# Performance work log

Measured on AMD Instinct MI355X. Metric: run time of the kernel, lower is better.

## Reference

```python
import jax, jax.numpy as jnp
import numpy as np

N = 6000        # nodes
F_IN = 300      # input feature dim
HID = 128       # per-head hidden dim
H = 8           # heads
NEG_INF = -9e15 # mask value used by dense GAT
ALPHA = 0.2     # LeakyReLU slope

# NOTE: dropout (p=0.6) is applied in torch only when training=True; this
# reference implements eval mode, so all dropouts are identity.

def setup_inputs() -> dict:
    key = jax.random.key(0)
    k1, k2, k3, k4, k5, k6 = jax.random.split(key, 6)
    x = jax.random.normal(k1, (N, F_IN), dtype=jnp.float32)
    # sparse-ish 0/1 dense adjacency with self-loops (row-normalizable mask)
    adj = (jax.random.uniform(k2, (N, N)) < 0.05).astype(jnp.float32)
    adj = jnp.maximum(adj, jnp.eye(N, dtype=jnp.float32))
    # per-head params: W ~ xavier_uniform, a ~ xavier_uniform ([2*HID, 1])
    def xavier(k, shape):
        fan_in, fan_out = shape[-2], shape[-1]
        lim = jnp.sqrt(6.0 / (fan_in + fan_out)).astype(jnp.float32)
        return jax.random.uniform(k, shape, jnp.float32, -lim, lim)
    W_heads = xavier(k3, (H, F_IN, HID))          # 8 attention heads
    a_heads = xavier(k4, (H, 2 * HID, 1))
    W_out = xavier(k5, (H * HID, HID))            # final GAT layer
    a_out = xavier(k6, (2 * HID, 1))
    return {"x": x, "adj": adj, "W_heads": W_heads, "a_heads": a_heads,
            "W_out": W_out, "a_out": a_out}


def _masked_softmax(e, adj):
    # attention = softmax over rows, restricted to adj > 0
    return jax.nn.softmax(jnp.where(adj > 0, e, NEG_INF), axis=-1)


def reference(x, adj, W_heads, a_heads, W_out, a_out):
    # ---- multi-head dense GAT layer (concat=True) ----
    Wh = jnp.einsum('nf,hfo->hno', x, W_heads)                    # [H,N,O]
    a1 = a_heads[:, :HID, 0]                                      # [H,O]
    a2 = a_heads[:, HID:, 0]                                      # [H,O]
    f1 = jnp.einsum('hno,ho->hn', Wh, a1)                         # [H,N]
    f2 = jnp.einsum('hno,ho->hn', Wh, a2)                         # [H,N]
    e = jax.nn.leaky_relu(f1[:, :, None] + f2[:, None, :], ALPHA) # [H,N,N]
    attn = _masked_softmax(e, adj[None])                          # [H,N,N]
    h = jax.nn.elu(jnp.einsum('hnm,hmo->hno', attn, Wh))          # [H,N,O]
    hcat = jnp.transpose(h, (1, 0, 2)).reshape(N, H * HID)        # [N,H*O]

    # ---- final GAT layer (concat=False, no elu) ----
    Wh2 = hcat @ W_out                                            # [N,O]
    g1 = (Wh2 @ a_out[:HID]).squeeze(-1)                          # [N]
    g2 = (Wh2 @ a_out[HID:]).squeeze(-1)                          # [N]
    e2 = jax.nn.leaky_relu(g1[:, None] + g2[None, :], ALPHA)      # [N,N]
    attn2 = _masked_softmax(e2, adj)                              # [N,N]
    out = attn2 @ Wh2                                             # [N,O]
    return out
```

## Files before the change

### kernel.cpp

```cpp
#include <hip/hip_runtime.h>
#include <hip/hip_fp16.h>
#include <math.h>

#define N 6000
#define FIN 300
#define HID 128
#define NH 8
#define ALPHA 0.2f
#define NBR_CAP 512
#define KSPLIT 4

typedef unsigned short u16;
typedef unsigned int u32;
typedef short bf16x8 __attribute__((ext_vector_type(8)));
typedef float f32x4 __attribute__((ext_vector_type(4)));

static __device__ __forceinline__ u16 f2bf(float f) {
    u32 u = __float_as_uint(f);
    u32 r = (u + 0x7fff + ((u >> 16) & 1)) >> 16;
    return (u16)r;
}
static __device__ __forceinline__ u16 f2h(float f) {
    return __half_as_ushort(__float2half(f));
}

__global__ void build_nbr(const float* __restrict__ adj,
                          u16* __restrict__ nbr,
                          int* __restrict__ ncnt) {
    int n = blockIdx.x;
    int t = threadIdx.x;
    int lane = t & 63, w = t >> 6;
    __shared__ u16 lbuf[4][256];
    __shared__ int wc[4];
    const int seg = N / 4;
    int start = w * seg, end = start + seg;
    const float* row = adj + (size_t)n * N;
    int cnt = 0;
    for (int base = start; base < end; base += 256) {
        int m0 = base + 4 * lane;
        float4 v = make_float4(0.f, 0.f, 0.f, 0.f);
        if (m0 < end) v = *(const float4*)(row + m0);
#pragma unroll
        for (int c = 0; c < 4; c++) {
            float vc = (c == 0) ? v.x : (c == 1) ? v.y : (c == 2) ? v.z : v.w;
            bool p = vc > 0.5f;
            unsigned long long mask = __ballot(p);
            if (p) {
                int pos = cnt + __popcll(mask & ((1ull << lane) - 1ull));
                if (pos < 256) lbuf[w][pos] = (u16)(m0 + c);
            }
            cnt += __popcll(mask);
        }
    }
    if (cnt > 256) cnt = 256;
    if (lane == 0) wc[w] = cnt;
    __syncthreads();
    int offset = 0;
    for (int i = 0; i < w; i++) offset += wc[i];
    for (int i = lane; i < cnt; i += 64) {
        int idx = offset + i;
        if (idx < NBR_CAP) nbr[(size_t)n * NBR_CAP + idx] = lbuf[w][i];
    }
    if (t == 0) {
        int total = wc[0] + wc[1] + wc[2] + wc[3];
        ncnt[n] = total < NBR_CAP ? total : NBR_CAP;
    }
}

__global__ void gemm_wh(const float* __restrict__ x,
                        const float* __restrict__ W,
                        const float* __restrict__ a_heads,
                        u16* __restrict__ Whb,
                        float* __restrict__ f1, float* __restrict__ f2) {
    int h = blockIdx.y;
    int n0 = blockIdx.x * 64;
    __shared__ float xs[64][21];
    __shared__ float bs[20][128];
    int t = threadIdx.x;
    int tx = t & 31, ty = t >> 5;
    float acc[8][4] = {};
    for (int k0 = 0; k0 < FIN; k0 += 20) {
        for (int i = t; i < 64 * 20; i += 256) {
            int r = i / 20, c = i - r * 20;
            int n = n0 + r;
            xs[r][c] = (n < N) ? x[(size_t)n * FIN + k0 + c] : 0.f;
        }
        for (int i = t; i < 20 * 128; i += 256) {
            int r = i >> 7, c = i & 127;
            bs[r][c] = W[((size_t)h * FIN + (k0 + r)) * HID + c];
        }
        __syncthreads();
#pragma unroll
        for (int kk = 0; kk < 20; kk++) {
            float b[4];
#pragma unroll
            for (int j = 0; j < 4; j++) b[j] = bs[kk][tx * 4 + j];
#pragma unroll
            for (int i = 0; i < 8; i++) {
                float a = xs[ty * 8 + i][kk];
#pragma unroll
                for (int j = 0; j < 4; j++) acc[i][j] += a * b[j];
            }
        }
        __syncthreads();
    }
    float a1c[4], a2c[4];
#pragma unroll
    for (int j = 0; j < 4; j++) {
        a1c[j] = a_heads[(size_t)h * 2 * HID + tx * 4 + j];
        a2c[j] = a_heads[(size_t)h * 2 * HID + HID + tx * 4 + j];
    }
    for (int i = 0; i < 8; i++) {
        int n = n0 + ty * 8 + i;
        float s1 = 0.f, s2 = 0.f;
#pragma unroll
        for (int j = 0; j < 4; j++) { s1 += acc[i][j] * a1c[j]; s2 += acc[i][j] * a2c[j]; }
        for (int d = 1; d <= 16; d <<= 1) { s1 += __shfl_xor(s1, d); s2 += __shfl_xor(s2, d); }
        if (n < N) {
            size_t ro = ((size_t)h * N + n) * HID + tx * 4;
            ushort4 b4;
            b4.x = f2bf(acc[i][0]); b4.y = f2bf(acc[i][1]);
            b4.z = f2bf(acc[i][2]); b4.w = f2bf(acc[i][3]);
            *(ushort4*)(Whb + ro) = b4;
            if (tx == 0) { f1[h * N + n] = s1; f2[h * N + n] = s2; }
        }
    }
}

__global__ void prep_wout(const float* __restrict__ W_out,
                          u16* __restrict__ WoT) {
    int idx = blockIdx.x * 256 + threadIdx.x;
    int k = idx & 1023, c = idx >> 10;
    WoT[(size_t)c * 1024 + k] = f2bf(W_out[(size_t)k * HID + c]);
}

__global__ void gat1(const u16* __restrict__ Whb,
                     const float* __restrict__ f1, const float* __restrict__ f2,
                     const u16* __restrict__ nbr,
                     const int* __restrict__ ncnt,
                     u16* __restrict__ hcatb) {
    int bid = blockIdx.x;
    int h = bid / N, n = bid - h * N;
    int t = threadIdx.x;
    int s = t >> 4, op = t & 15;
    int cnt = ncnt[n];
    const u16* lst = nbr + (size_t)n * NBR_CAP;
    __shared__ float2 wm[NBR_CAP];
    __shared__ float accl[16][16][9];
    __shared__ float swl[16];

    float f1c = f1[h * N + n];
    for (int i = t; i < cnt; i += 256) {
        int m = lst[i];
        float z = f1c + f2[h * N + m];
        z = (z >= 0.f) ? z : ALPHA * z;
        wm[i] = make_float2(__expf(z), __uint_as_float((u32)m << 8));
    }
    __syncthreads();

    const char* base = (const char*)(Whb + (size_t)h * N * HID) + (op << 4);
    float acc[8] = {};
    float sw = 0.f;
    int j = s;
    for (; j + 16 < cnt; j += 32) {
        float2 p0 = wm[j];
        float2 p1 = wm[j + 16];
        const uint4 va = *(const uint4*)(base + __float_as_uint(p0.y));
        const uint4 vb = *(const uint4*)(base + __float_as_uint(p1.y));
        float w0 = p0.x, w1 = p1.x;
        acc[0] += w0 * __uint_as_float(va.x << 16);
        acc[1] += w0 * __uint_as_float(va.x);
        acc[2] += w0 * __uint_as_float(va.y << 16);
        acc[3] += w0 * __uint_as_float(va.y);
        acc[4] += w0 * __uint_as_float(va.z << 16);
        acc[5] += w0 * __uint_as_float(va.z);
        acc[6] += w0 * __uint_as_float(va.w << 16);
        acc[7] += w0 * __uint_as_float(va.w);
        acc[0] += w1 * __uint_as_float(vb.x << 16);
        acc[1] += w1 * __uint_as_float(vb.x);
        acc[2] += w1 * __uint_as_float(vb.y << 16);
        acc[3] += w1 * __uint_as_float(vb.y);
        acc[4] += w1 * __uint_as_float(vb.z << 16);
        acc[5] += w1 * __uint_as_float(vb.z);
        acc[6] += w1 * __uint_as_float(vb.w << 16);
        acc[7] += w1 * __uint_as_float(vb.w);
        sw += w0 + w1;
    }
    if (j < cnt) {
        float2 p0 = wm[j];
        const uint4 va = *(const uint4*)(base + __float_as_uint(p0.y));
        float w0 = p0.x;
        acc[0] += w0 * __uint_as_float(va.x << 16);
        acc[1] += w0 * __uint_as_float(va.x);
        acc[2] += w0 * __uint_as_float(va.y << 16);
        acc[3] += w0 * __uint_as_float(va.y);
        acc[4] += w0 * __uint_as_float(va.z << 16);
        acc[5] += w0 * __uint_as_float(va.z);
        acc[6] += w0 * __uint_as_float(va.w << 16);
        acc[7] += w0 * __uint_as_float(va.w);
        sw += w0;
    }
#pragma unroll
    for (int c = 0; c < 8; c++) accl[s][op][c] = acc[c];
    if (op == 0) swl[s] = sw;
    __syncthreads();

    if (t < 128) {
        int c = t;
        float r = 0.f;
#pragma unroll
        for (int k = 0; k < 16; k++) r += accl[k][c >> 3][c & 7];
        float swt = 0.f;
#pragma unroll
        for (int k = 0; k < 16; k++) swt += swl[k];
        r /= swt;
        r = (r > 0.f) ? r : expm1f(r);
        hcatb[(size_t)n * (NH * HID) + h * HID + c] = f2bf(r);
    }
}

__global__ __launch_bounds__(256)
void gemm_out_mfma(const u16* __restrict__ hcatb,
                   const u16* __restrict__ WoT,
                   float* __restrict__ partial) {
    int n0 = blockIdx.x * 64;
    int ks = blockIdx.y;
    int t = threadIdx.x;
    int lane = t & 63, wid = t >> 6;
    int l4 = lane >> 4, lr = lane & 15;

    __shared__ u16 Bt[128][128];

    f32x4 acc[8];
#pragma unroll
    for (int ct = 0; ct < 8; ct++) acc[ct] = (f32x4){0.f, 0.f, 0.f, 0.f};

    int arow = n0 + 16 * wid + lr;
    const u16* asrc = hcatb + (size_t)arow * (NH * HID);
    bool avalid = (arow < N);

    for (int half = 0; half < 2; half++) {
        int kbeg = ks * 256 + half * 128;
        {
            int c = t >> 1, sh = t & 1;
            const u16* src = WoT + (size_t)c * 1024 + kbeg + sh * 64;
            int cx = (c & 7) << 3;
            uint4 v[8];
#pragma unroll
            for (int j = 0; j < 8; j++) v[j] = ((const uint4*)src)[j];
#pragma unroll
            for (int j = 0; j < 8; j++)
                *(uint4*)&Bt[c][(sh * 64 + 8 * j) ^ cx] = v[j];
        }
        __syncthreads();
#pragma unroll
        for (int kst = 0; kst < 4; kst++) {
            int kb = kst * 32 + 8 * l4;
            bf16x8 a = {0, 0, 0, 0, 0, 0, 0, 0};
            if (avalid) a = *(const bf16x8*)(asrc + kbeg + kb);
#pragma unroll
            for (int ct = 0; ct < 8; ct++) {
                int brow = 16 * ct + lr;
                bf16x8 b = *(const bf16x8*)&Bt[brow][kb ^ ((brow & 7) << 3)];
                acc[ct] = __builtin_amdgcn_mfma_f32_16x16x32_bf16(a, b, acc[ct], 0, 0, 0);
            }
        }
        __syncthreads();
    }
    float* pout = partial + (size_t)ks * N * HID;
#pragma unroll
    for (int reg = 0; reg < 4; reg++) {
        int n = n0 + 16 * wid + 4 * l4 + reg;
        if (n < N) {
#pragma unroll
            for (int ct = 0; ct < 8; ct++)
                pout[(size_t)n * HID + 16 * ct + lr] = acc[ct][reg];
        }
    }
}

__global__ void reduce_wh2(const float* __restrict__ partial,
                           const float* __restrict__ a_out,
                           u16* __restrict__ Wh2h,
                           float* __restrict__ g1, float* __restrict__ g2) {
    int idx = blockIdx.x * 256 + threadIdx.x;
    float4 v = *(const float4*)(partial + 4 * (size_t)idx);
#pragma unroll
    for (int s = 1; s < KSPLIT; s++) {
        const float4 q = *(const float4*)(partial + (size_t)s * N * HID + 4 * (size_t)idx);
        v.x += q.x; v.y += q.y; v.z += q.z; v.w += q.w;
    }
    ushort4 h4;
    h4.x = f2h(v.x); h4.y = f2h(v.y); h4.z = f2h(v.z); h4.w = f2h(v.w);
    *(ushort4*)(Wh2h + 4 * (size_t)idx) = h4;

    int row = idx >> 5, cg = idx & 31;
    float p1 = v.x * a_out[4 * cg] + v.y * a_out[4 * cg + 1]
             + v.z * a_out[4 * cg + 2] + v.w * a_out[4 * cg + 3];
    float p2 = v.x * a_out[HID + 4 * cg] + v.y * a_out[HID + 4 * cg + 1]
             + v.z * a_out[HID + 4 * cg + 2] + v.w * a_out[HID + 4 * cg + 3];
    for (int d = 1; d <= 16; d <<= 1) { p1 += __shfl_xor(p1, d); p2 += __shfl_xor(p2, d); }
    if ((threadIdx.x & 31) == 0) { g1[row] = p1; g2[row] = p2; }
}

__global__ void gat2(const u16* __restrict__ Wh2h,
                     const float* __restrict__ g1, const float* __restrict__ g2,
                     const u16* __restrict__ nbr,
                     const int* __restrict__ ncnt,
                     float* __restrict__ out) {
    int n = blockIdx.x, t = threadIdx.x;
    int s = t >> 4, op = t & 15;
    int cnt = ncnt[n];
    const u16* lst = nbr + (size_t)n * NBR_CAP;
    __shared__ float2 wm[NBR_CAP];
    __shared__ float accl[16][16][9];
    __shared__ float swl[16];

    float g1c = g1[n];
    for (int i = t; i < cnt; i += 256) {
        int m = lst[i];
        float z = g1c + g2[m];
        z = (z >= 0.f) ? z : ALPHA * z;
        wm[i] = make_float2(__expf(z), __uint_as_float((u32)m << 8));
    }
    __syncthreads();

    const char* base = (const char*)Wh2h + (op << 4);
    float acc[8] = {};
    float sw = 0.f;
    int j = s;
    for (; j + 16 < cnt; j += 32) {
        float2 p0 = wm[j];
        float2 p1 = wm[j + 16];
        const uint4 va = *(const uint4*)(base + __float_as_uint(p0.y));
        const uint4 vb = *(const uint4*)(base + __float_as_uint(p1.y));
        float w0 = p0.x, w1 = p1.x;
        acc[0] += w0 * __half2float(__ushort_as_half((u16)(va.x & 0xffff)));
        acc[1] += w0 * __half2float(__ushort_as_half((u16)(va.x >> 16)));
        acc[2] += w0 * __half2float(__ushort_as_half((u16)(va.y & 0xffff)));
        acc[3] += w0 * __half2float(__ushort_as_half((u16)(va.y >> 16)));
        acc[4] += w0 * __half2float(__ushort_as_half((u16)(va.z & 0xffff)));
        acc[5] += w0 * __half2float(__ushort_as_half((u16)(va.z >> 16)));
        acc[6] += w0 * __half2float(__ushort_as_half((u16)(va.w & 0xffff)));
        acc[7] += w0 * __half2float(__ushort_as_half((u16)(va.w >> 16)));
        acc[0] += w1 * __half2float(__ushort_as_half((u16)(vb.x & 0xffff)));
        acc[1] += w1 * __half2float(__ushort_as_half((u16)(vb.x >> 16)));
        acc[2] += w1 * __half2float(__ushort_as_half((u16)(vb.y & 0xffff)));
        acc[3] += w1 * __half2float(__ushort_as_half((u16)(vb.y >> 16)));
        acc[4] += w1 * __half2float(__ushort_as_half((u16)(vb.z & 0xffff)));
        acc[5] += w1 * __half2float(__ushort_as_half((u16)(vb.z >> 16)));
        acc[6] += w1 * __half2float(__ushort_as_half((u16)(vb.w & 0xffff)));
        acc[7] += w1 * __half2float(__ushort_as_half((u16)(vb.w >> 16)));
        sw += w0 + w1;
    }
    if (j < cnt) {
        float2 p0 = wm[j];
        const uint4 va = *(const uint4*)(base + __float_as_uint(p0.y));
        float w0 = p0.x;
        acc[0] += w0 * __half2float(__ushort_as_half((u16)(va.x & 0xffff)));
        acc[1] += w0 * __half2float(__ushort_as_half((u16)(va.x >> 16)));
        acc[2] += w0 * __half2float(__ushort_as_half((u16)(va.y & 0xffff)));
        acc[3] += w0 * __half2float(__ushort_as_half((u16)(va.y >> 16)));
        acc[4] += w0 * __half2float(__ushort_as_half((u16)(va.z & 0xffff)));
        acc[5] += w0 * __half2float(__ushort_as_half((u16)(va.z >> 16)));
        acc[6] += w0 * __half2float(__ushort_as_half((u16)(va.w & 0xffff)));
        acc[7] += w0 * __half2float(__ushort_as_half((u16)(va.w >> 16)));
        sw += w0;
    }
#pragma unroll
    for (int c = 0; c < 8; c++) accl[s][op][c] = acc[c];
    if (op == 0) swl[s] = sw;
    __syncthreads();

    if (t < 128) {
        int c = t;
        float r = 0.f;
#pragma unroll
        for (int k = 0; k < 16; k++) r += accl[k][c >> 3][c & 7];
        float swt = 0.f;
#pragma unroll
        for (int k = 0; k < 16; k++) swt += swl[k];
        out[(size_t)n * HID + c] = r / swt;
    }
}

extern "C" void kernel_launch(void* const* d_in, const int* in_sizes, int n_in,
                              void* d_out, int out_size, void* d_ws, size_t ws_size,
                              hipStream_t stream) {
    const float* x       = (const float*)d_in[0];
    const float* adj     = (const float*)d_in[1];
    const float* W_heads = (const float*)d_in[2];
    const float* a_heads = (const float*)d_in[3];
    const float* W_out   = (const float*)d_in[4];
    const float* a_out   = (const float*)d_in[5];
    float* out = (float*)d_out;

    char* wsb = (char*)d_ws;
    size_t off = 0;
    auto alloc = [&](size_t bytes) {
        void* p = wsb + off;
        off += (bytes + 255) & ~(size_t)255;
        return p;
    };
    float* partial = (float*)alloc(sizeof(float) * (size_t)KSPLIT * N * HID);
    u16*   Whb  = (u16*)  alloc(sizeof(u16)   * (size_t)NH * N * HID);
    u16*   hcatb= (u16*)  alloc(sizeof(u16)   * (size_t)N * NH * HID);
    u16*   WoT  = (u16*)  alloc(sizeof(u16)   * (size_t)HID * 1024);
    u16*   Wh2h = (u16*)  alloc(sizeof(u16)   * (size_t)N * HID);
    float* f1   = (float*)alloc(sizeof(float) * (size_t)NH * N);
    float* f2   = (float*)alloc(sizeof(float) * (size_t)NH * N);
    float* g1   = (float*)alloc(sizeof(float) * (size_t)N);
    float* g2   = (float*)alloc(sizeof(float) * (size_t)N);
    u16* nbr    = (u16*)  alloc(sizeof(u16)   * (size_t)N * NBR_CAP);
    int* ncnt   = (int*)  alloc(sizeof(int)   * (size_t)N);

    hipLaunchKernelGGL(build_nbr, dim3(N), dim3(256), 0, stream, adj, nbr, ncnt);
    hipLaunchKernelGGL(gemm_wh, dim3((N + 63) / 64, NH), dim3(256), 0, stream,
                       x, W_heads, a_heads, Whb, f1, f2);
    hipLaunchKernelGGL(prep_wout, dim3(512), dim3(256), 0, stream, W_out, WoT);
    hipLaunchKernelGGL(gat1, dim3(NH * N), dim3(256), 0, stream, Whb, f1, f2, nbr, ncnt, hcatb);
    hipLaunchKernelGGL(gemm_out_mfma, dim3((N + 63) / 64, KSPLIT), dim3(256), 0, stream,
                       hcatb, WoT, partial);
    hipLaunchKernelGGL(reduce_wh2, dim3(N * HID / 4 / 256), dim3(256), 0, stream,
                       partial, a_out, Wh2h, g1, g2);
    hipLaunchKernelGGL(gat2, dim3(N), dim3(256), 0, stream, Wh2h, g1, g2, nbr, ncnt, out);
}
```

Before: 321.2 us.

## Move first-layer projection GEMM to bf16 MFMA with precomputed attention vectors

Replaces the fp32 SIMT GEMM for x·W_heads with a bf16 MFMA kernel over padded, pre-converted and transposed operands held in swizzled LDS. The f1/f2 attention logits are now computed separately as x·(W·a) through a small precomputed vector per head, so they no longer depend on the GEMM epilogue. The W_out prep is folded into one combined prep kernel. This aims to cut first-layer GEMM time, at the cost of extra conversion passes, an additional launch and bf16 rounding of the x input.

```diff
diff --git a/kernel.cpp b/kernel.cpp
--- a/kernel.cpp
+++ b/kernel.cpp
@@ -9,6 +9,7 @@
 #define ALPHA 0.2f
 #define NBR_CAP 512
 #define KSPLIT 4
+#define KPAD 384
 
 typedef unsigned short u16;
 typedef unsigned int u32;
@@ -67,71 +68,134 @@
     }
 }
 
-__global__ void gemm_wh(const float* __restrict__ x,
-                        const float* __restrict__ W,
-                        const float* __restrict__ a_heads,
-                        u16* __restrict__ Whb,
-                        float* __restrict__ f1, float* __restrict__ f2) {
+__global__ void prep_all(const float* __restrict__ x,
+                         const float* __restrict__ W,
+                         const float* __restrict__ W_out,
+                         const float* __restrict__ a_heads,
+                         u16* __restrict__ xb,
+                         u16* __restrict__ WbT,
+                         u16* __restrict__ WoT,
+                         float* __restrict__ av1, float* __restrict__ av2) {
+    int bid = blockIdx.x, t = threadIdx.x;
+    if (bid < 9000) {
+        int idx = bid * 256 + t;
+        int n = idx / KPAD, k = idx - n * KPAD;
+        xb[idx] = (k < FIN) ? f2bf(x[(size_t)n * FIN + k]) : (u16)0;
+    } else if (bid < 9000 + 1536) {
+        int idx = (bid - 9000) * 256 + t;
+        int k = idx % KPAD;
+        int c = (idx / KPAD) & 127;
+        int h = idx / (KPAD * HID);
+        WbT[idx] = (k < FIN) ? f2bf(W[((size_t)h * FIN + k) * HID + c]) : (u16)0;
+    } else if (bid < 9000 + 1536 + 512) {
+        int idx = (bid - 9000 - 1536) * 256 + t;
+        int k = idx & 1023, c = idx >> 10;
+        WoT[idx] = f2bf(W_out[(size_t)k * HID + c]);
+    } else {
+        int h = bid - (9000 + 1536 + 512);
+        __shared__ float a1s[HID], a2s[HID];
+        if (t < HID) {
+            a1s[t] = a_heads[(size_t)h * 2 * HID + t];
+            a2s[t] = a_heads[(size_t)h * 2 * HID + HID + t];
+        }
+        __syncthreads();
+        for (int f = t; f < 320; f += 256) {
+            float s1 = 0.f, s2 = 0.f;
+            if (f < FIN) {
+                const float* wr = W + ((size_t)h * FIN + f) * HID;
+#pragma unroll 4
+                for (int o = 0; o < HID; o++) { s1 += wr[o] * a1s[o]; s2 += wr[o] * a2s[o]; }
+            }
+            av1[h * 320 + f] = s1;
+            av2[h * 320 + f] = s2;
+        }
+    }
+}
+
+__global__ void calc_f(const float* __restrict__ x,
+                       const float* __restrict__ av1, const float* __restrict__ av2,
+                       float* __restrict__ f1, float* __restrict__ f2) {
+    int n = blockIdx.x, t = threadIdx.x;
+    int lane = t & 63, w = t >> 6;
+    __shared__ float xsh[320];
+    for (int i = t; i < 320; i += 256)
+        xsh[i] = (i < FIN) ? x[(size_t)n * FIN + i] : 0.f;
+    __syncthreads();
+#pragma unroll
+    for (int hh = 0; hh < 2; hh++) {
+        int h = 2 * w + hh;
+        const float* a1 = av1 + h * 320;
+        const float* a2 = av2 + h * 320;
+        float s1 = 0.f, s2 = 0.f;
+#pragma unroll
+        for (int i = 0; i < 5; i++) {
+            float xv = xsh[lane + 64 * i];
+            s1 += xv * a1[lane + 64 * i];
+            s2 += xv * a2[lane + 64 * i];
+        }
+        for (int d = 1; d <= 32; d <<= 1) { s1 += __shfl_xor(s1, d); s2 += __shfl_xor(s2, d); }
+        if (lane == 0) { f1[h * N + n] = s1; f2[h * N + n] = s2; }
+    }
+}
+
+__global__ __launch_bounds__(256)
+void gemm_wh_mfma(const u16* __restrict__ xb,
+                  const u16* __restrict__ WbT,
+                  u16* __restrict__ Whb) {
+    int n0 = blockIdx.x * 64;
     int h = blockIdx.y;
-    int n0 = blockIdx.x * 64;
-    __shared__ float xs[64][21];
-    __shared__ float bs[20][128];
     int t = threadIdx.x;
-    int tx = t & 31, ty = t >> 5;
-    float acc[8][4] = {};
-    for (int k0 = 0; k0 < FIN; k0 += 20) {
-        for (int i = t; i < 64 * 20; i += 256) {
-            int r = i / 20, c = i - r * 20;
-            int n = n0 + r;
-            xs[r][c] = (n < N) ? x[(size_t)n * FIN + k0 + c] : 0.f;
-        }
-        for (int i = t; i < 20 * 128; i += 256) {
-            int r = i >> 7, c = i & 127;
-            bs[r][c] = W[((size_t)h * FIN + (k0 + r)) * HID + c];
+    int lane = t & 63, wid = t >> 6;
+    int l4 = lane >> 4, lr = lane & 15;
+
+    __shared__ u16 Bt[128][128];
+
+    f32x4 acc[8];
+#pragma unroll
+    for (int ct = 0; ct < 8; ct++) acc[ct] = (f32x4){0.f, 0.f, 0.f, 0.f};
+
+    int arow = n0 + 16 * wid + lr;
+    const u16* asrc = xb + (size_t)arow * KPAD;
+    bool avalid = (arow < N);
+
+    for (int half = 0; half < 3; half++) {
+        int kbeg = half * 128;
+        {
+            int c = t >> 1, sh = t & 1;
+            const u16* src = WbT + ((size_t)h * HID + c) * KPAD + kbeg + sh * 64;
+            int cx = (c & 7) << 3;
+            uint4 v[8];
+#pragma unroll
+            for (int j = 0; j < 8; j++) v[j] = ((const uint4*)src)[j];
+#pragma unroll
+            for (int j = 0; j < 8; j++)
+                *(uint4*)&Bt[c][(sh * 64 + 8 * j) ^ cx] = v[j];
         }
         __syncthreads();
 #pragma unroll
-        for (int kk = 0; kk < 20; kk++) {
-            float b[4];
-#pragma unroll
-            for (int j = 0; j < 4; j++) b[j] = bs[kk][tx * 4 + j];
-#pragma unroll
-            for (int i = 0; i < 8; i++) {
-                float a = xs[ty * 8 + i][kk];
-#pragma unroll
-                for (int j = 0; j < 4; j++) acc[i][j] += a * b[j];
+        for (int kst = 0; kst < 4; kst++) {
+            int kb = kst * 32 + 8 * l4;
+            bf16x8 a = {0, 0, 0, 0, 0, 0, 0, 0};
+            if (avalid) a = *(const bf16x8*)(asrc + kbeg + kb);
+#pragma unroll
+            for (int ct = 0; ct < 8; ct++) {
+                int brow = 16 * ct + lr;
+                bf16x8 b = *(const bf16x8*)&Bt[brow][kb ^ ((brow & 7) << 3)];
+                acc[ct] = __builtin_amdgcn_mfma_f32_16x16x32_bf16(a, b, acc[ct], 0, 0, 0);
             }
         }
         __syncthreads();
     }
-    float a1c[4], a2c[4];
-#pragma unroll
-    for (int j = 0; j < 4; j++) {
-        a1c[j] = a_heads[(size_t)h * 2 * HID + tx * 4 + j];
-        a2c[j] = a_heads[(size_t)h * 2 * HID + HID + tx * 4 + j];
-    }
-    for (int i = 0; i < 8; i++) {
-        int n = n0 + ty * 8 + i;
-        float s1 = 0.f, s2 = 0.f;
-#pragma unroll
-        for (int j = 0; j < 4; j++) { s1 += acc[i][j] * a1c[j]; s2 += acc[i][j] * a2c[j]; }
-        for (int d = 1; d <= 16; d <<= 1) { s1 += __shfl_xor(s1, d); s2 += __shfl_xor(s2, d); }
+#pragma unroll
+    for (int reg = 0; reg < 4; reg++) {
+        int n = n0 + 16 * wid + 4 * l4 + reg;
         if (n < N) {
-            size_t ro = ((size_t)h * N + n) * HID + tx * 4;
-            ushort4 b4;
-            b4.x = f2bf(acc[i][0]); b4.y = f2bf(acc[i][1]);
-            b4.z = f2bf(acc[i][2]); b4.w = f2bf(acc[i][3]);
-            *(ushort4*)(Whb + ro) = b4;
-            if (tx == 0) { f1[h * N + n] = s1; f2[h * N + n] = s2; }
-        }
-    }
-}
-
-__global__ void prep_wout(const float* __restrict__ W_out,
-                          u16* __restrict__ WoT) {
-    int idx = blockIdx.x * 256 + threadIdx.x;
-    int k = idx & 1023, c = idx >> 10;
-    WoT[(size_t)c * 1024 + k] = f2bf(W_out[(size_t)k * HID + c]);
+            u16* orow = Whb + ((size_t)h * N + n) * HID;
+#pragma unroll
+            for (int ct = 0; ct < 8; ct++)
+                orow[16 * ct + lr] = f2bf(acc[ct][reg]);
+        }
+    }
 }
 
 __global__ void gat1(const u16* __restrict__ Whb,
@@ -405,8 +469,12 @@
     float* partial = (float*)alloc(sizeof(float) * (size_t)KSPLIT * N * HID);
     u16*   Whb  = (u16*)  alloc(sizeof(u16)   * (size_t)NH * N * HID);
     u16*   hcatb= (u16*)  alloc(sizeof(u16)   * (size_t)N * NH * HID);
+    u16*   xb   = (u16*)  alloc(sizeof(u16)   * (size_t)N * KPAD);
+    u16*   WbT  = (u16*)  alloc(sizeof(u16)   * (size_t)NH * HID * KPAD);
     u16*   WoT  = (u16*)  alloc(sizeof(u16)   * (size_t)HID * 1024);
     u16*   Wh2h = (u16*)  alloc(sizeof(u16)   * (size_t)N * HID);
+    float* av1  = (float*)alloc(sizeof(float) * (size_t)NH * 320);
+    float* av2  = (float*)alloc(sizeof(float) * (size_t)NH * 320);
     float* f1   = (float*)alloc(sizeof(float) * (size_t)NH * N);
     float* f2   = (float*)alloc(sizeof(float) * (size_t)NH * N);
     float* g1   = (float*)alloc(sizeof(float) * (size_t)N);
@@ -415,9 +483,11 @@
     int* ncnt   = (int*)  alloc(sizeof(int)   * (size_t)N);
 
     hipLaunchKernelGGL(build_nbr, dim3(N), dim3(256), 0, stream, adj, nbr, ncnt);
-    hipLaunchKernelGGL(gemm_wh, dim3((N + 63) / 64, NH), dim3(256), 0, stream,
-                       x, W_heads, a_heads, Whb, f1, f2);
-    hipLaunchKernelGGL(prep_wout, dim3(512), dim3(256), 0, stream, W_out, WoT);
+    hipLaunchKernelGGL(prep_all, dim3(9000 + 1536 + 512 + 8), dim3(256), 0, stream,
+                       x, W_heads, W_out, a_heads, xb, WbT, WoT, av1, av2);
+    hipLaunchKernelGGL(calc_f, dim3(N), dim3(256), 0, stream, x, av1, av2, f1, f2);
+    hipLaunchKernelGGL(gemm_wh_mfma, dim3((N + 63) / 64, NH), dim3(256), 0, stream,
+                       xb, WbT, Whb);
     hipLaunchKernelGGL(gat1, dim3(NH * N), dim3(256), 0, stream, Whb, f1, f2, nbr, ncnt, hcatb);
     hipLaunchKernelGGL(gemm_out_mfma, dim3((N + 63) / 64, KSPLIT), dim3(256), 0, stream,
                        hcatb, WoT, partial);
```

New measurement: 281.5 us. 12.4% less time.
